# Optimization experiments

Hardware: AMD Instinct MI355X
Metric: run time of the kernel (lower is better)

Reference implementation:

```python
import jax, jax.numpy as jnp
import numpy as np

N = 1_000_000
D = 128
CLS = 2


def setup_inputs() -> dict:
    key = jax.random.key(0)
    k1, k2, k3 = jax.random.split(key, 3)
    f = jax.random.normal(k1, (N, D), dtype=jnp.float32)
    center = jax.random.normal(k2, (CLS, D), dtype=jnp.float32)
    t = jax.random.randint(k3, (N,), 0, CLS, dtype=jnp.int64)
    return {"f": f, "center": center, "t": t}


def reference(f, center, t):
    # gather per-sample centers: [N, D]
    c = center[t]
    # L2 distance per sample: [N]
    d = jnp.sqrt(jnp.sum((f - c) ** 2, axis=-1))
    # histc(t, bins=2, min=0, max=1) over integer labels {0,1} == bincount
    h = jnp.bincount(t, length=CLS)
    # per-sample class count, normalize and sum -> scalar
    n = h[t].astype(f.dtype)
    return jnp.sum(d / n)
```

## Files before the change

kernel.cpp:

```cpp
#include <hip/hip_runtime.h>
#include <math.h>

#define BLOCK 256
#define GROUPS_PER_BLOCK (BLOCK / 32)

__global__ __launch_bounds__(BLOCK, 4) void center_loss_main(
    const float* __restrict__ f,
    const float* __restrict__ center,
    const int* __restrict__ t,
    float* __restrict__ ws,
    int N)
{
    const int lane = threadIdx.x & 31;
    const int grp  = threadIdx.x >> 5;
    const int groups_total = gridDim.x * GROUPS_PER_BLOCK;
    const int g0 = blockIdx.x * GROUPS_PER_BLOCK + grp;

    const float4* __restrict__ f4 = (const float4*)f;
    const float4* __restrict__ c4 = (const float4*)center;
    const float4 c0 = c4[lane];
    const float4 c1 = c4[32 + lane];

    float sum0 = 0.f, sum1 = 0.f, cnt0 = 0.f, cnt1 = 0.f;

    for (int s = g0; s < N; s += groups_total) {
        const int cls = t[s];
        const float4 fv = f4[s * 32 + lane];
        const float4 cv = (cls == 0) ? c0 : c1;
        const float dx = fv.x - cv.x;
        const float dy = fv.y - cv.y;
        const float dz = fv.z - cv.z;
        const float dw = fv.w - cv.w;
        float ss = dx * dx + dy * dy + dz * dz + dw * dw;
        ss += __shfl_down(ss, 16, 32);
        ss += __shfl_down(ss, 8, 32);
        ss += __shfl_down(ss, 4, 32);
        ss += __shfl_down(ss, 2, 32);
        ss += __shfl_down(ss, 1, 32);
        if (lane == 0) {
            const float d = sqrtf(ss);
            if (cls == 0) { sum0 += d; cnt0 += 1.f; }
            else          { sum1 += d; cnt1 += 1.f; }
        }
    }

    __shared__ float ls[4][GROUPS_PER_BLOCK];
    if (lane == 0) {
        ls[0][grp] = sum0;
        ls[1][grp] = sum1;
        ls[2][grp] = cnt0;
        ls[3][grp] = cnt1;
    }
    __syncthreads();
    if (threadIdx.x < 4) {
        float v = 0.f;
#pragma unroll
        for (int i = 0; i < GROUPS_PER_BLOCK; ++i) v += ls[threadIdx.x][i];
        atomicAdd(&ws[threadIdx.x], v);
    }
}

__global__ void center_loss_final(const float* __restrict__ ws,
                                  float* __restrict__ out)
{
    const float s0 = ws[0], s1 = ws[1], c0 = ws[2], c1 = ws[3];
    float r = 0.f;
    if (c0 > 0.f) r += s0 / c0;
    if (c1 > 0.f) r += s1 / c1;
    out[0] = r;
}

extern "C" void kernel_launch(void* const* d_in, const int* in_sizes, int n_in,
                              void* d_out, int out_size, void* d_ws, size_t ws_size,
                              hipStream_t stream)
{
    const float* f      = (const float*)d_in[0];
    const float* center = (const float*)d_in[1];
    const int*   t      = (const int*)d_in[2];
    float* out = (float*)d_out;
    float* ws  = (float*)d_ws;

    const int N = in_sizes[0] / 128;

    hipMemsetAsync(ws, 0, 4 * sizeof(float), stream);

    const int grid = 2048;
    center_loss_main<<<grid, BLOCK, 0, stream>>>(f, center, t, ws, N);
    center_loss_final<<<1, 1, 0, stream>>>(ws, out);
}
```

Before: 649.1 us.

## Unroll sample loop by two, use nontemporal loads, fuse final reduction via last-block

The main loop now handles two samples per iteration so more loads are in flight per wave, and it reads features with nontemporal loads to avoid polluting the cache on a pure streaming pass. The separate finalize kernel is removed: a completion counter in the workspace lets the last block compute the output, which saves one kernel launch. Launch bounds are raised to allow more waves per CU. In exchange the code needs threadfence and atomic-counter logic, and it relies on the grid size matching the compile-time constant.

```diff
diff --git a/kernel.cpp b/kernel.cpp
--- a/kernel.cpp
+++ b/kernel.cpp
@@ -3,34 +3,67 @@
 
 #define BLOCK 256
 #define GROUPS_PER_BLOCK (BLOCK / 32)
+#define GRID 2048
 
-__global__ __launch_bounds__(BLOCK, 4) void center_loss_main(
+typedef float f32x4 __attribute__((ext_vector_type(4)));
+
+__global__ __launch_bounds__(BLOCK, 8) void center_loss_main(
     const float* __restrict__ f,
     const float* __restrict__ center,
     const int* __restrict__ t,
     float* __restrict__ ws,
+    float* __restrict__ out,
     int N)
 {
     const int lane = threadIdx.x & 31;
     const int grp  = threadIdx.x >> 5;
-    const int groups_total = gridDim.x * GROUPS_PER_BLOCK;
+    const int stride = GRID * GROUPS_PER_BLOCK;
     const int g0 = blockIdx.x * GROUPS_PER_BLOCK + grp;
 
-    const float4* __restrict__ f4 = (const float4*)f;
+    const f32x4* __restrict__ f4 = (const f32x4*)f;
     const float4* __restrict__ c4 = (const float4*)center;
     const float4 c0 = c4[lane];
     const float4 c1 = c4[32 + lane];
 
     float sum0 = 0.f, sum1 = 0.f, cnt0 = 0.f, cnt1 = 0.f;
 
-    for (int s = g0; s < N; s += groups_total) {
+    int s = g0;
+    for (; s + stride < N; s += 2 * stride) {
+        const int sA = s, sB = s + stride;
+        const int clsA = t[sA];
+        const int clsB = t[sB];
+        const f32x4 fvA = __builtin_nontemporal_load(&f4[sA * 32 + lane]);
+        const f32x4 fvB = __builtin_nontemporal_load(&f4[sB * 32 + lane]);
+        const float4 cvA = (clsA == 0) ? c0 : c1;
+        const float4 cvB = (clsB == 0) ? c0 : c1;
+
+        float dxA = fvA.x - cvA.x, dyA = fvA.y - cvA.y;
+        float dzA = fvA.z - cvA.z, dwA = fvA.w - cvA.w;
+        float ssA = dxA * dxA + dyA * dyA + dzA * dzA + dwA * dwA;
+
+        float dxB = fvB.x - cvB.x, dyB = fvB.y - cvB.y;
+        float dzB = fvB.z - cvB.z, dwB = fvB.w - cvB.w;
+        float ssB = dxB * dxB + dyB * dyB + dzB * dzB + dwB * dwB;
+
+        ssA += __shfl_down(ssA, 16, 32);  ssB += __shfl_down(ssB, 16, 32);
+        ssA += __shfl_down(ssA, 8, 32);   ssB += __shfl_down(ssB, 8, 32);
+        ssA += __shfl_down(ssA, 4, 32);   ssB += __shfl_down(ssB, 4, 32);
+        ssA += __shfl_down(ssA, 2, 32);   ssB += __shfl_down(ssB, 2, 32);
+        ssA += __shfl_down(ssA, 1, 32);   ssB += __shfl_down(ssB, 1, 32);
+
+        if (lane == 0) {
+            const float dA = sqrtf(ssA);
+            const float dB = sqrtf(ssB);
+            if (clsA == 0) { sum0 += dA; cnt0 += 1.f; } else { sum1 += dA; cnt1 += 1.f; }
+            if (clsB == 0) { sum0 += dB; cnt0 += 1.f; } else { sum1 += dB; cnt1 += 1.f; }
+        }
+    }
+    for (; s < N; s += stride) {
         const int cls = t[s];
-        const float4 fv = f4[s * 32 + lane];
+        const f32x4 fv = __builtin_nontemporal_load(&f4[s * 32 + lane]);
         const float4 cv = (cls == 0) ? c0 : c1;
-        const float dx = fv.x - cv.x;
-        const float dy = fv.y - cv.y;
-        const float dz = fv.z - cv.z;
-        const float dw = fv.w - cv.w;
+        const float dx = fv.x - cv.x, dy = fv.y - cv.y;
+        const float dz = fv.z - cv.z, dw = fv.w - cv.w;
         float ss = dx * dx + dy * dy + dz * dz + dw * dw;
         ss += __shfl_down(ss, 16, 32);
         ss += __shfl_down(ss, 8, 32);
@@ -39,8 +72,7 @@
         ss += __shfl_down(ss, 1, 32);
         if (lane == 0) {
             const float d = sqrtf(ss);
-            if (cls == 0) { sum0 += d; cnt0 += 1.f; }
-            else          { sum1 += d; cnt1 += 1.f; }
+            if (cls == 0) { sum0 += d; cnt0 += 1.f; } else { sum1 += d; cnt1 += 1.f; }
         }
     }
 
@@ -58,16 +90,23 @@
         for (int i = 0; i < GROUPS_PER_BLOCK; ++i) v += ls[threadIdx.x][i];
         atomicAdd(&ws[threadIdx.x], v);
     }
-}
+    __syncthreads();
 
-__global__ void center_loss_final(const float* __restrict__ ws,
-                                  float* __restrict__ out)
-{
-    const float s0 = ws[0], s1 = ws[1], c0 = ws[2], c1 = ws[3];
-    float r = 0.f;
-    if (c0 > 0.f) r += s0 / c0;
-    if (c1 > 0.f) r += s1 / c1;
-    out[0] = r;
+    if (threadIdx.x == 0) {
+        __threadfence();
+        const unsigned old = atomicAdd((unsigned*)&ws[4], 1u);
+        if (old == (unsigned)(GRID - 1)) {
+            __threadfence();
+            const float s0 = atomicAdd(&ws[0], 0.f);
+            const float s1 = atomicAdd(&ws[1], 0.f);
+            const float c0r = atomicAdd(&ws[2], 0.f);
+            const float c1r = atomicAdd(&ws[3], 0.f);
+            float r = 0.f;
+            if (c0r > 0.f) r += s0 / c0r;
+            if (c1r > 0.f) r += s1 / c1r;
+            out[0] = r;
+        }
+    }
 }
 
 extern "C" void kernel_launch(void* const* d_in, const int* in_sizes, int n_in,
@@ -82,9 +121,7 @@
 
     const int N = in_sizes[0] / 128;
 
-    hipMemsetAsync(ws, 0, 4 * sizeof(float), stream);
+    hipMemsetAsync(ws, 0, 8 * sizeof(float), stream);
 
-    const int grid = 2048;
-    center_loss_main<<<grid, BLOCK, 0, stream>>>(f, center, t, ws, N);
-    center_loss_final<<<1, 1, 0, stream>>>(ws, out);
+    center_loss_main<<<GRID, BLOCK, 0, stream>>>(f, center, t, ws, out, N);
 }
```

Measured after the change: 704.7 us. +8.6%, slower.
